# Optimization experiments

Measured on AMD Instinct MI355X. Metric: run time of the kernel, lower is better.

The kernel has to match this reference:

```python
import jax, jax.numpy as jnp
import numpy as np

EPS = 1e-5

def _ln(x, g, b):
    m = jnp.mean(x, axis=-1, keepdims=True)
    v = jnp.var(x, axis=-1, keepdims=True)
    return (x - m) / jnp.sqrt(v + EPS) * g + b

def setup_inputs() -> dict:
    key = jax.random.key(0)
    ks = jax.random.split(key, 16)
    B, T, N, K, d, E = 2, 12, 512, 8, 64, 64
    D = K * d
    s = 0.02
    inp = {
        "x": jax.random.normal(ks[0], (B, T, N, D), jnp.float32),
        "lapmatrix": jax.random.normal(ks[1], (N, N), jnp.float32),
        "node_embeddings": jax.random.normal(ks[2], (N, E), jnp.float32),
        "Wq": jax.random.normal(ks[3], (D, D), jnp.float32) * s,
        "bq": jnp.zeros((D,), jnp.float32),
        "Wk": jax.random.normal(ks[4], (D, D), jnp.float32) * s,
        "bk": jnp.zeros((D,), jnp.float32),
        "Wv": jax.random.normal(ks[5], (D, D), jnp.float32) * s,
        "bv": jnp.zeros((D,), jnp.float32),
        "Wo": jax.random.normal(ks[6], (D, D), jnp.float32) * s,
        "bo": jnp.zeros((D,), jnp.float32),
        "W1": jax.random.normal(ks[7], (4 * D, D), jnp.float32) * s,
        "b1": jnp.zeros((4 * D,), jnp.float32),
        "W2": jax.random.normal(ks[8], (D, 4 * D), jnp.float32) * s,
        "b2": jnp.zeros((D,), jnp.float32),
        "g1": jnp.ones((D,), jnp.float32),
        "be1": jnp.zeros((D,), jnp.float32),
        "g2": jnp.ones((D,), jnp.float32),
        "be2": jnp.zeros((D,), jnp.float32),
        "alpha": jnp.float32(1.0),
        "beta": jnp.float32(1.0),
        "k": 3,
    }
    return inp

def reference(x, lapmatrix, node_embeddings, Wq, bq, Wk, bk, Wv, bv, Wo, bo,
              W1, b1, W2, b2, g1, be1, g2, be2, alpha, beta, k):
    B, T, N, D = x.shape
    K, d = 8, D // 8
    x_raw = x
    xn = _ln(x, g1, be1)
    q = (xn @ Wq.T + bq).reshape(B, T, N, K, d)
    kk = (xn @ Wk.T + bk).reshape(B, T, N, K, d)
    v = (xn @ Wv.T + bv).reshape(B, T, N, K, d)
    # raw attention logits: [B,T,K,N,N]
    raw = jnp.einsum('btnkd,btmkd->btknm', q, kk) / jnp.sqrt(jnp.float32(d))
    # graph biases, all [N,N], broadcast over B,T,K
    supports = jax.nn.softmax(jax.nn.relu(node_embeddings @ node_embeddings.T), axis=1)
    adj = (lapmatrix != 0).astype(x.dtype)
    mask = jnp.where(adj == 0, jnp.float32(-1e9), jnp.float32(0.0))
    logits = raw + alpha * supports + beta * lapmatrix + mask
    attn = jax.nn.softmax(logits, axis=-1)  # dropout = identity in eval
    out = jnp.einsum('btknm,btmkd->btnkd', attn, v).reshape(B, T, N, D)
    x1 = x_raw + (out @ Wo.T + bo)
    h = _ln(x1, g2, be2)
    ffn = jax.nn.relu(h @ W1.T + b1) @ W2.T + b2
    return x1 + ffn
```

## Files before the change

kernel.cpp:

```cpp
#include <hip/hip_runtime.h>

typedef unsigned short u16;
typedef unsigned int   u32;
typedef __attribute__((ext_vector_type(8))) short bf16x8;
typedef __attribute__((ext_vector_type(4))) float f32x4;

#define DEV static __device__ __forceinline__

DEV float b2f(u16 u){ return __uint_as_float(((u32)u)<<16); }
DEV u16 f2b(float f){
  u32 u = __float_as_uint(f);
  u32 r = (u + 0x7FFFu + ((u>>16)&1u)) >> 16;
  return (u16)r;
}

union V8 { uint4 v; u16 s[8]; };

DEV u32 cvt_pk_bf16(float lo, float hi){
  u32 r;
  asm("v_cvt_pk_bf16_f32 %0, %1, %2" : "=v"(r) : "v"(lo), "v"(hi));
  return r;
}

DEV bool is_f32(const void* dt){ return *(const u32*)dt == 0x3F800000u; }

DEV uint4 ld8_ext_bf(const void* p, size_t i, bool f32){
  if(f32){
    const float* q = (const float*)p + i;
    float4 a = *(const float4*)q, b = *(const float4*)(q+4);
    V8 r;
    r.s[0]=f2b(a.x); r.s[1]=f2b(a.y); r.s[2]=f2b(a.z); r.s[3]=f2b(a.w);
    r.s[4]=f2b(b.x); r.s[5]=f2b(b.y); r.s[6]=f2b(b.z); r.s[7]=f2b(b.w);
    return r.v;
  }
  return *(const uint4*)((const u16*)p + i);
}
DEV void ld8_ext_f(const void* p, size_t i, bool f32, float* o){
  if(f32){
    const float* q = (const float*)p + i;
    float4 a = *(const float4*)q, b = *(const float4*)(q+4);
    o[0]=a.x;o[1]=a.y;o[2]=a.z;o[3]=a.w;o[4]=b.x;o[5]=b.y;o[6]=b.z;o[7]=b.w;
  }else{
    V8 u; u.v = *(const uint4*)((const u16*)p + i);
    #pragma unroll
    for(int k=0;k<8;k++) o[k]=b2f(u.s[k]);
  }
}
DEV float ld1_ext(const void* p, size_t i, bool f32){
  return f32 ? ((const float*)p)[i] : b2f(((const u16*)p)[i]);
}
DEV float load_scalar(const void* p, bool f32){
  return f32 ? *(const float*)p : b2f(*(const u16*)p);
}

DEV void gl_lds16(const u16* g, u16* l){
  __builtin_amdgcn_global_load_lds((const __attribute__((address_space(1))) void*)g,
                                   (__attribute__((address_space(3))) void*)l, 16, 0, 0);
}

__global__ __launch_bounds__(256) void sentinel_kernel(u16* out, long n, const void* dt){
  long ne = is_f32(dt) ? 2*n : n;
  long i = (long)blockIdx.x*256 + threadIdx.x;
  if(i < ne) out[i] = 0x4442;
}

__global__ __launch_bounds__(256) void prep_kernel(
    const void* __restrict__ x, const void* __restrict__ g1,
    const void* __restrict__ be1, u16* __restrict__ xn,
    const void* Wq, const void* Wk, const void* Wv, const void* Wo,
    const void* W1, const void* W2, u16* __restrict__ wbf,
    const void* bq, const void* bk, const void* bv, const void* bo,
    const void* b1, const void* b2, float* __restrict__ bfp,
    const void* __restrict__ E, const void* __restrict__ lap,
    const void* __restrict__ alpha_p, const void* __restrict__ beta_p,
    float* __restrict__ bm, const void* dt)
{
  __shared__ float En[64];
  __shared__ float red[8];
  const bool f32 = is_f32(dt);
  const int bid = blockIdx.x, t = threadIdx.x;

  if(bid < 3072){
    const int row = bid*4 + (t>>6), lane = t&63;
    float v[8];
    ld8_ext_f(x, (size_t)row*512 + lane*8, f32, v);
    float s=0.f, ss=0.f;
    #pragma unroll
    for(int i=0;i<8;i++){ s+=v[i]; ss+=v[i]*v[i]; }
    #pragma unroll
    for(int o=1;o<64;o<<=1){ s+=__shfl_xor(s,o,64); ss+=__shfl_xor(ss,o,64); }
    const float mean = s*(1.0f/512.0f);
    const float var  = ss*(1.0f/512.0f) - mean*mean;
    const float rstd = rsqrtf(var + 1e-5f);
    float gv[8], bv[8];
    ld8_ext_f(g1, (size_t)lane*8, f32, gv);
    ld8_ext_f(be1, (size_t)lane*8, f32, bv);
    V8 o8;
    #pragma unroll
    for(int i=0;i<8;i++) o8.s[i]=f2b((v[i]-mean)*rstd*gv[i]+bv[i]);
    *(uint4*)(xn+(size_t)row*512+lane*8)=o8.v;
  } else if(bid < 4608){
    size_t i = ((size_t)(bid-3072)*256 + t)*8;
    const void* src; size_t base;
    if(i < 262144){ src=Wq; base=0; }
    else if(i < 524288){ src=Wk; base=262144; }
    else if(i < 786432){ src=Wv; base=524288; }
    else if(i < 1048576){ src=Wo; base=786432; }
    else if(i < 2097152){ src=W1; base=1048576; }
    else { src=W2; base=2097152; }
    *(uint4*)(wbf + i) = ld8_ext_bf(src, i-base, f32);
  } else if(bid < 5120){
    const int n = bid - 4608;
    if(t < 64) En[t] = ld1_ext(E, (size_t)n*64 + t, f32);
    __syncthreads();
    const float alpha = load_scalar(alpha_p, f32);
    const float beta  = load_scalar(beta_p, f32);
    const int m0 = t, m1 = t+256;
    float sc0=0.f, sc1=0.f;
    #pragma unroll
    for(int c=0;c<8;c++){
      float a0[8], a1[8];
      ld8_ext_f(E, (size_t)m0*64 + c*8, f32, a0);
      ld8_ext_f(E, (size_t)m1*64 + c*8, f32, a1);
      #pragma unroll
      for(int j=0;j<8;j++){ const float en = En[c*8+j]; sc0 += en*a0[j]; sc1 += en*a1[j]; }
    }
    sc0 = fmaxf(sc0, 0.f); sc1 = fmaxf(sc1, 0.f);
    float mx = fmaxf(sc0, sc1);
    for(int o=1;o<64;o<<=1) mx = fmaxf(mx, __shfl_xor(mx,o,64));
    const int wave = t>>6;
    if((t&63)==0) red[wave]=mx;
    __syncthreads();
    mx = fmaxf(fmaxf(red[0],red[1]), fmaxf(red[2],red[3]));
    float e0 = __expf(sc0-mx), e1 = __expf(sc1-mx);
    float sm = e0+e1;
    for(int o=1;o<64;o<<=1) sm += __shfl_xor(sm,o,64);
    if((t&63)==0) red[4+wave]=sm;
    __syncthreads();
    sm = red[4]+red[5]+red[6]+red[7];
    const float inv = 1.f/sm;
    const int q0b = n>>5, iq = (n>>4)&1, l16 = n&15;
    const size_t qpart = (size_t)q0b*256 + (size_t)l16*4 + iq;
    float lv0 = ld1_ext(lap, (size_t)n*512+m0, f32);
    {
      float val = alpha*e0*inv + beta*lv0 + (lv0==0.f ? -1e9f : 0.f);
      int kb = m0>>3, e = m0&7;
      bm[(size_t)kb*4096 + qpart + (e>>1)*64 + (e&1)*2] = val;
    }
    float lv1 = ld1_ext(lap, (size_t)n*512+m1, f32);
    {
      float val = alpha*e1*inv + beta*lv1 + (lv1==0.f ? -1e9f : 0.f);
      int kb = m1>>3, e = m1&7;
      bm[(size_t)kb*4096 + qpart + (e>>1)*64 + (e&1)*2] = val;
    }
  } else {
    int j = (bid-5120)*256 + t;
    const void* src; int off;
    if(j < 512){ src=bq; off=0; }
    else if(j < 1024){ src=bk; off=512; }
    else if(j < 1536){ src=bv; off=1024; }
    else if(j < 2048){ src=bo; off=1536; }
    else if(j < 4096){ src=b1; off=2048; }
    else { src=b2; off=4096; }
    bfp[j] = ld1_ext(src, j-off, f32);
  }
}

template<int EXTIN>
__global__ __launch_bounds__(64) void ln_kernel(const void* __restrict__ xin,
    const void* __restrict__ g, const void* __restrict__ b, u16* __restrict__ out,
    const void* dt)
{
  const bool f32 = is_f32(dt);
  const int row = blockIdx.x, lane = threadIdx.x;
  float v[8];
  if(EXTIN){
    ld8_ext_f(xin, (size_t)row*512 + lane*8, f32, v);
  }else{
    V8 u; u.v = *(const uint4*)((const u16*)xin + (size_t)row*512 + lane*8);
    #pragma unroll
    for(int i=0;i<8;i++) v[i]=b2f(u.s[i]);
  }
  float s=0.f, ss=0.f;
  #pragma unroll
  for(int i=0;i<8;i++){ s+=v[i]; ss+=v[i]*v[i]; }
  #pragma unroll
  for(int o=1;o<64;o<<=1){ s+=__shfl_xor(s,o,64); ss+=__shfl_xor(ss,o,64); }
  const float mean = s*(1.0f/512.0f);
  const float var  = ss*(1.0f/512.0f) - mean*mean;
  const float rstd = rsqrtf(var + 1e-5f);
  float gv[8], bv[8];
  ld8_ext_f(g, (size_t)lane*8, f32, gv);
  ld8_ext_f(b, (size_t)lane*8, f32, bv);
  V8 o8;
  #pragma unroll
  for(int i=0;i<8;i++) o8.s[i]=f2b((v[i]-mean)*rstd*gv[i]+bv[i]);
  *(uint4*)(out+(size_t)row*512+lane*8)=o8.v;
}

template<int RELU, int RES, int RESEXT, int OUTEXT>
__global__ __launch_bounds__(256) void gemm_nt(
    const u16* __restrict__ A, const u16* __restrict__ B,
    const float* __restrict__ bias, const void* __restrict__ resid,
    void* __restrict__ Cout, int N, int K, const void* dt)
{
  __shared__ u16 As[128*64];
  __shared__ u16 Bs[128*64];
  const bool f32 = is_f32(dt);
  const int t = threadIdx.x;
  const int wave = t>>6, lane = t&63;
  const int n0 = blockIdx.y*128, m0 = blockIdx.x*128;
  const int wr = wave>>1, wc = wave&1;

  f32x4 acc[4][4];
  #pragma unroll
  for(int i=0;i<4;i++)
    #pragma unroll
    for(int j=0;j<4;j++){ acc[i][j][0]=0.f; acc[i][j][1]=0.f; acc[i][j][2]=0.f; acc[i][j][3]=0.f; }

  const int lrow8 = lane>>3, lg = lane&7;
  const int gsw = (lg ^ lrow8)*8;
  const u16* Ag = A + (size_t)(m0+lrow8)*K + gsw;
  const u16* Bg = B + (size_t)(n0+lrow8)*K + gsw;
  const int fr = lane&15, qd = lane>>4, frk = (fr&7);

  for(int k0=0; k0<K; k0+=64){
    __syncthreads();
    #pragma unroll
    for(int i=0;i<4;i++){
      int c = wave*4+i;
      gl_lds16(Ag + (size_t)(c*8)*K + k0, &As[c*512]);
      gl_lds16(Bg + (size_t)(c*8)*K + k0, &Bs[c*512]);
    }
    __syncthreads();
    #pragma unroll
    for(int s=0;s<2;s++){
      const int slot = ((s*4+qd) ^ frk)*8;
      bf16x8 af[4], bfr[4];
      #pragma unroll
      for(int i=0;i<4;i++) af[i] = *(const bf16x8*)&As[(wr*64+i*16+fr)*64 + slot];
      #pragma unroll
      for(int j=0;j<4;j++) bfr[j] = *(const bf16x8*)&Bs[(wc*64+j*16+fr)*64 + slot];
      #pragma unroll
      for(int i=0;i<4;i++)
        #pragma unroll
        for(int j=0;j<4;j++)
          acc[i][j] = __builtin_amdgcn_mfma_f32_16x16x32_bf16(af[i], bfr[j], acc[i][j], 0,0,0);
    }
  }

  const int col16 = lane&15, rbase = (lane>>4)*4;
  #pragma unroll
  for(int i=0;i<4;i++){
    #pragma unroll
    for(int j=0;j<4;j++){
      const int gc = n0 + wc*64 + j*16 + col16;
      const float bv = bias[gc];
      #pragma unroll
      for(int r=0;r<4;r++){
        const int gr = m0 + wr*64 + i*16 + rbase + r;
        float val = acc[i][j][r] + bv;
        if(RELU) val = fmaxf(val, 0.f);
        if(RES){
          if(RESEXT) val += ld1_ext(resid, (size_t)gr*N+gc, f32);
          else       val += b2f(((const u16*)resid)[(size_t)gr*N+gc]);
        }
        if(OUTEXT && f32) ((float*)Cout)[(size_t)gr*N+gc] = val;
        else              ((u16*)Cout)[(size_t)gr*N+gc] = f2b(val);
      }
    }
  }
}

template<int RELU, int RES, int RESEXT, int OUTEXT>
__global__ __launch_bounds__(256) void gemm_nt64(
    const u16* __restrict__ A, const u16* __restrict__ B,
    const float* __restrict__ bias, const void* __restrict__ resid,
    void* __restrict__ Cout, int N, int K, const void* dt)
{
  __shared__ u16 As[128*64];
  __shared__ u16 Bs[64*64];
  const bool f32 = is_f32(dt);
  const int t = threadIdx.x;
  const int wave = t>>6, lane = t&63;
  const int n0 = blockIdx.y*64, m0 = blockIdx.x*128;
  const int wr = wave>>1, wc = wave&1;

  f32x4 acc[4][2];
  #pragma unroll
  for(int i=0;i<4;i++)
    #pragma unroll
    for(int j=0;j<2;j++){ acc[i][j][0]=0.f; acc[i][j][1]=0.f; acc[i][j][2]=0.f; acc[i][j][3]=0.f; }

  const int lrow8 = lane>>3, lg = lane&7;
  const int gsw = (lg ^ lrow8)*8;
  const u16* Ag = A + (size_t)(m0+lrow8)*K + gsw;
  const u16* Bg = B + (size_t)(n0+lrow8)*K + gsw;
  const int fr = lane&15, qd = lane>>4, frk = (fr&7);

  for(int k0=0; k0<K; k0+=64){
    __syncthreads();
    #pragma unroll
    for(int i=0;i<4;i++){
      int c = wave*4+i;
      gl_lds16(Ag + (size_t)(c*8)*K + k0, &As[c*512]);
    }
    #pragma unroll
    for(int i=0;i<2;i++){
      int c = wave*2+i;
      gl_lds16(Bg + (size_t)(c*8)*K + k0, &Bs[c*512]);
    }
    __syncthreads();
    #pragma unroll
    for(int s=0;s<2;s++){
      const int slot = ((s*4+qd) ^ frk)*8;
      bf16x8 af[4], bfr[2];
      #pragma unroll
      for(int i=0;i<4;i++) af[i] = *(const bf16x8*)&As[(wr*64+i*16+fr)*64 + slot];
      #pragma unroll
      for(int j=0;j<2;j++) bfr[j] = *(const bf16x8*)&Bs[(wc*32+j*16+fr)*64 + slot];
      #pragma unroll
      for(int i=0;i<4;i++)
        #pragma unroll
        for(int j=0;j<2;j++)
          acc[i][j] = __builtin_amdgcn_mfma_f32_16x16x32_bf16(af[i], bfr[j], acc[i][j], 0,0,0);
    }
  }

  const int col16 = lane&15, rbase = (lane>>4)*4;
  #pragma unroll
  for(int i=0;i<4;i++){
    #pragma unroll
    for(int j=0;j<2;j++){
      const int gc = n0 + wc*32 + j*16 + col16;
      const float bv = bias[gc];
      #pragma unroll
      for(int r=0;r<4;r++){
        const int gr = m0 + wr*64 + i*16 + rbase + r;
        float val = acc[i][j][r] + bv;
        if(RELU) val = fmaxf(val, 0.f);
        if(RES){
          if(RESEXT) val += ld1_ext(resid, (size_t)gr*N+gc, f32);
          else       val += b2f(((const u16*)resid)[(size_t)gr*N+gc]);
        }
        if(OUTEXT && f32) ((float*)Cout)[(size_t)gr*N+gc] = val;
        else              ((u16*)Cout)[(size_t)gr*N+gc] = f2b(val);
      }
    }
  }
}

__global__ __launch_bounds__(256,3) void attn_kernel(
    const u16* __restrict__ qkv, const float* __restrict__ bm,
    u16* __restrict__ out)
{
  __shared__ u16 Kb[128*64];
  __shared__ u16 Vt[2][64*136];

  const int QS = 1536;
  const int t = threadIdx.x, wave = t>>6, lane = t&63;
  const int head = blockIdx.x, bt = blockIdx.z;
  const int q0 = blockIdx.y*128 + wave*32;
  const u16* qp = qkv + (size_t)bt*512*QS + head*64;
  const u16* kp = qp + 512;
  const u16* vp = qp + 1024;

  const int l16 = lane&15, qd = lane>>4;

  const int lrow8 = lane>>3, lg = lane&7;
  const int srow = t & 127;
  const int shalf = (t >> 7) * 32;
  const u16* vcp = vp + (size_t)srow*QS + shalf;

  #pragma unroll
  for(int ii=0;ii<4;ii++){
    const int c8 = wave*4 + ii;
    const int pg = lg ^ ((2*(lrow8&3) + (c8&3)) & 7);
    gl_lds16(kp + (size_t)(c8*8 + lrow8)*QS + pg*8, &Kb[c8*512]);
  }
  uint4 vv[4];
  #pragma unroll
  for(int qi=0;qi<4;qi++) vv[qi] = *(const uint4*)(vcp + qi*8);

  bf16x8 qf[2][2];
  #pragma unroll
  for(int i=0;i<2;i++)
    #pragma unroll
    for(int kc=0;kc<2;kc++)
      qf[i][kc] = *(const bf16x8*)(qp + (size_t)(q0 + i*16 + l16)*QS + kc*32 + qd*8);

  const float* bml = bm + (size_t)(blockIdx.y*4 + wave)*256 + (size_t)qd*4096 + (size_t)l16*4;

  const int arow = ((l16>>2)<<3) + (l16&3);
  const int rperm = (2*(l16&3) + (l16>>2)) & 7;
  const int g0 = (qd ^ rperm)*8;
  const u16* KA0 = &Kb[arow*64 + g0];
  const u16* KA1 = &Kb[arow*64 + (g0 ^ 32)];

  float mrun[2], lrun[2];
  mrun[0] = -3e38f; mrun[1] = -3e38f;
  lrun[0] = 0.f;    lrun[1] = 0.f;
  f32x4 oacc[2][4];
  #pragma unroll
  for(int i=0;i<2;i++)
    #pragma unroll
    for(int j=0;j<4;j++){ oacc[i][j][0]=0.f; oacc[i][j][1]=0.f; oacc[i][j][2]=0.f; oacc[i][j][3]=0.f; }

  #pragma unroll
  for(int qi=0;qi<4;qi++){
    V8 u; u.v = vv[qi];
    #pragma unroll
    for(int jj=0;jj<8;jj++) Vt[0][(shalf + qi*8 + jj)*136 + srow] = u.s[jj];
  }
  __syncthreads();

  #pragma unroll
  for(int c=0;c<4;c++){
    f32x4 p[2][8];
    __builtin_amdgcn_s_setprio(1);
    #pragma unroll
    for(int tt=0;tt<8;tt++){
      const int ro = (tt&3)*2048 + (tt>>2)*256;
      bf16x8 a0 = *(const bf16x8*)(KA0 + ro);
      bf16x8 a1 = *(const bf16x8*)(KA1 + ro);
      #pragma unroll
      for(int i=0;i<2;i++){
        f32x4 s; s[0]=0.f; s[1]=0.f; s[2]=0.f; s[3]=0.f;
        s = __builtin_amdgcn_mfma_f32_16x16x32_bf16(a0, qf[i][0], s, 0,0,0);
        s = __builtin_amdgcn_mfma_f32_16x16x32_bf16(a1, qf[i][1], s, 0,0,0);
        p[i][tt] = s;
      }
    }
    __builtin_amdgcn_s_setprio(0);
    if(c<3){
      __syncthreads();
      #pragma unroll
      for(int ii=0;ii<4;ii++){
        const int c8 = wave*4 + ii;
        const int pg = lg ^ ((2*(lrow8&3) + (c8&3)) & 7);
        gl_lds16(kp + (size_t)((c+1)*128 + c8*8 + lrow8)*QS + pg*8, &Kb[c8*512]);
      }
      #pragma unroll
      for(int qi=0;qi<4;qi++) vv[qi] = *(const uint4*)(vcp + (size_t)((c+1)*128)*QS + qi*8);
    }

    float mx0 = -3e38f, mx1 = -3e38f;
    #pragma unroll
    for(int s4=0;s4<4;s4++){
      const float* bp = bml + c*65536 + s4*16384;
      const float4 bg0 = *(const float4*)(bp);
      const float4 bg1 = *(const float4*)(bp + 64);
      const float4 bg2 = *(const float4*)(bp + 128);
      const float4 bg3 = *(const float4*)(bp + 192);
      #pragma unroll
      for(int i=0;i<2;i++){
        f32x4& pl = p[i][s4];
        pl[0] = pl[0]*0.125f + (i ? bg0.y : bg0.x);
        pl[1] = pl[1]*0.125f + (i ? bg0.w : bg0.z);
        pl[2] = pl[2]*0.125f + (i ? bg1.y : bg1.x);
        pl[3] = pl[3]*0.125f + (i ? bg1.w : bg1.z);
        f32x4& ph = p[i][s4+4];
        ph[0] = ph[0]*0.125f + (i ? bg2.y : bg2.x);
        ph[1] = ph[1]*0.125f + (i ? bg2.w : bg2.z);
        ph[2] = ph[2]*0.125f + (i ? bg3.y : bg3.x);
        ph[3] = ph[3]*0.125f + (i ? bg3.w : bg3.z);
        const float m8 = fmaxf(fmaxf(fmaxf(pl[0],pl[1]),fmaxf(pl[2],pl[3])),
                               fmaxf(fmaxf(ph[0],ph[1]),fmaxf(ph[2],ph[3])));
        if(i==0) mx0 = fmaxf(mx0, m8); else mx1 = fmaxf(mx1, m8);
      }
    }

    #pragma unroll
    for(int i=0;i<2;i++){
      float mx = i ? mx1 : mx0;
      mx = fmaxf(mx, __shfl_xor(mx, 16, 64));
      mx = fmaxf(mx, __shfl_xor(mx, 32, 64));
      const float mnew = fmaxf(mrun[i], mx);
      if(__any(mx > mrun[i])){
        const float al = __expf(mrun[i] - mnew);
        lrun[i] *= al;
        #pragma unroll
        for(int r=0;r<4;r++){
          const float alr = __shfl(al, (qd<<2)+r, 64);
          #pragma unroll
          for(int j=0;j<4;j++) oacc[i][j][r] *= alr;
        }
      }
      mrun[i] = mnew;
      float rs = 0.f;
      #pragma unroll
      for(int tt=0;tt<8;tt++){
        p[i][tt][0] = __expf(p[i][tt][0]-mnew);
        p[i][tt][1] = __expf(p[i][tt][1]-mnew);
        p[i][tt][2] = __expf(p[i][tt][2]-mnew);
        p[i][tt][3] = __expf(p[i][tt][3]-mnew);
        rs += (p[i][tt][0]+p[i][tt][1]) + (p[i][tt][2]+p[i][tt][3]);
      }
      rs += __shfl_xor(rs, 16, 64);
      rs += __shfl_xor(rs, 32, 64);
      lrun[i] += rs;
    }

    __builtin_amdgcn_s_setprio(1);
    #pragma unroll
    for(int ks=0;ks<4;ks++){
      union { bf16x8 v; u32 w[4]; } pa[2];
      #pragma unroll
      for(int i=0;i<2;i++){
        pa[i].w[0] = cvt_pk_bf16(p[i][ks][0],   p[i][ks][1]);
        pa[i].w[1] = cvt_pk_bf16(p[i][ks][2],   p[i][ks][3]);
        pa[i].w[2] = cvt_pk_bf16(p[i][ks+4][0], p[i][ks+4][1]);
        pa[i].w[3] = cvt_pk_bf16(p[i][ks+4][2], p[i][ks+4][3]);
      }
      #pragma unroll
      for(int j=0;j<4;j++){
        bf16x8 bvf = *(const bf16x8*)&Vt[c&1][(j*16 + l16)*136 + ks*32 + qd*8];
        oacc[0][j] = __builtin_amdgcn_mfma_f32_16x16x32_bf16(pa[0].v, bvf, oacc[0][j], 0,0,0);
        oacc[1][j] = __builtin_amdgcn_mfma_f32_16x16x32_bf16(pa[1].v, bvf, oacc[1][j], 0,0,0);
      }
    }
    __builtin_amdgcn_s_setprio(0);

    if(c<3){
      #pragma unroll
      for(int qi=0;qi<4;qi++){
        V8 u; u.v = vv[qi];
        #pragma unroll
        for(int jj=0;jj<8;jj++) Vt[(c+1)&1][(shalf + qi*8 + jj)*136 + srow] = u.s[jj];
      }
      __syncthreads();
    }
  }

  u16* op = out + (size_t)bt*512*512 + head*64;
  #pragma unroll
  for(int i=0;i<2;i++){
    const float inv = 1.f / lrun[i];
    #pragma unroll
    for(int r=0;r<4;r++){
      const float invr = __shfl(inv, (qd<<2)+r, 64);
      const size_t rowb = (size_t)(q0 + i*16 + qd*4 + r)*512;
      #pragma unroll
      for(int j=0;j<4;j++)
        op[rowb + j*16 + l16] = f2b(oacc[i][j][r] * invr);
    }
  }
}

extern "C" void kernel_launch(void* const* d_in, const int* in_sizes, int n_in,
                              void* d_out, int out_size, void* d_ws, size_t ws_size,
                              hipStream_t stream) {
  const void* x   = d_in[0];
  const void* lap = d_in[1];
  const void* ne  = d_in[2];
  const void* Wq  = d_in[3];
  const void* bq  = d_in[4];
  const void* Wk  = d_in[5];
  const void* bk  = d_in[6];
  const void* Wv  = d_in[7];
  const void* bv  = d_in[8];
  const void* Wo  = d_in[9];
  const void* bo  = d_in[10];
  const void* W1  = d_in[11];
  const void* b1  = d_in[12];
  const void* W2  = d_in[13];
  const void* b2  = d_in[14];
  const void* g1  = d_in[15];
  const void* be1 = d_in[16];
  const void* g2  = d_in[17];
  const void* be2 = d_in[18];
  const void* alpha = d_in[19];
  const void* beta  = d_in[20];
  const void* dt = g1;

  const int M = 12288;
  const size_t NEED = (size_t)512*512*4 + (size_t)M*512*2*2 + (size_t)M*2048*2
                    + (size_t)3145728*2 + (size_t)4608*4;
  if(ws_size < NEED){
    long n = out_size;
    sentinel_kernel<<<(2*n+255)/256, 256, 0, stream>>>((u16*)d_out, n, dt);
    return;
  }
  char* w = (char*)d_ws;
  float* bias_m = (float*)w;              w += (size_t)512*512*4;
  u16*   slotB  = (u16*)w;                w += (size_t)M*512*2;
  char*  slotC  = w;                      w += (size_t)M*2048*2;
  u16*   x1     = (u16*)w;                w += (size_t)M*512*2;
  u16*   wbf    = (u16*)w;                w += (size_t)3145728*2;
  float* bfp    = (float*)w;
  u16* qkv = (u16*)slotC;
  u16* h1  = (u16*)slotC;
  u16* xn = slotB;
  u16* ao = slotB;
  u16* h  = slotB;

  prep_kernel<<<5138, 256, 0, stream>>>(
      x, g1, be1, xn,
      Wq, Wk, Wv, Wo, W1, W2, wbf,
      bq, bk, bv, bo, b1, b2, bfp,
      ne, lap, alpha, beta, bias_m, dt);
  gemm_nt<0,0,0,0><<<dim3(96,12), 256, 0, stream>>>(xn, wbf, bfp, nullptr, qkv, 1536, 512, dt);
  attn_kernel<<<dim3(8,4,24), 256, 0, stream>>>(qkv, bias_m, ao);
  gemm_nt64<0,1,1,0><<<dim3(96,8), 256, 0, stream>>>(ao, wbf+786432, bfp+1536, x, x1, 512, 512, dt);
  ln_kernel<0><<<M, 64, 0, stream>>>(x1, g2, be2, h, dt);
  gemm_nt<1,0,0,0><<<dim3(96,16), 256, 0, stream>>>(h, wbf+1048576, bfp+2048, nullptr, h1, 2048, 512, dt);
  gemm_nt64<0,1,0,1><<<dim3(96,8), 256, 0, stream>>>(h1, wbf+2097152, bfp+4096, x1, d_out, 512, 2048, dt);
}
```

Before: 328.3 us.

## Double-buffer GEMM LDS tiles with K=32 steps and MFMA priority boost

```diff
diff --git a/kernel.cpp b/kernel.cpp
--- a/kernel.cpp
+++ b/kernel.cpp
@@ -204,8 +204,8 @@
     const float* __restrict__ bias, const void* __restrict__ resid,
     void* __restrict__ Cout, int N, int K, const void* dt)
 {
-  __shared__ u16 As[128*64];
-  __shared__ u16 Bs[128*64];
+  __shared__ u16 As[2][128*32];
+  __shared__ u16 Bs[2][128*32];
   const bool f32 = is_f32(dt);
   const int t = threadIdx.x;
   const int wave = t>>6, lane = t&63;
@@ -218,35 +218,51 @@
     #pragma unroll
     for(int j=0;j<4;j++){ acc[i][j][0]=0.f; acc[i][j][1]=0.f; acc[i][j][2]=0.f; acc[i][j][3]=0.f; }
 
-  const int lrow8 = lane>>3, lg = lane&7;
-  const int gsw = (lg ^ lrow8)*8;
-  const u16* Ag = A + (size_t)(m0+lrow8)*K + gsw;
-  const u16* Bg = B + (size_t)(n0+lrow8)*K + gsw;
-  const int fr = lane&15, qd = lane>>4, frk = (fr&7);
-
-  for(int k0=0; k0<K; k0+=64){
+  const int lrow16 = lane>>2, lg = lane&3;
+  const int pgsw = (lg ^ ((lrow16>>1)&3))*8;
+  const u16* Ag = A + (size_t)(m0+lrow16)*K + pgsw;
+  const u16* Bg = B + (size_t)(n0+lrow16)*K + pgsw;
+
+  const int fr = lane&15, qd = lane>>4;
+  const int slot = (qd ^ ((fr>>1)&3))*8;
+  const int aoff = (wr*64+fr)*32 + slot;
+  const int boff = (wc*64+fr)*32 + slot;
+
+  const int nt = K>>5;
+  #pragma unroll
+  for(int ii=0;ii<2;ii++){
+    const int c = wave*2+ii;
+    gl_lds16(Ag + (size_t)(c*16)*K, &As[0][c*512]);
+    gl_lds16(Bg + (size_t)(c*16)*K, &Bs[0][c*512]);
+  }
+  __syncthreads();
+
+  for(int tk=0; tk<nt; ++tk){
+    const int cur = tk&1;
+    if(tk+1 < nt){
+      const int k0 = (tk+1)*32;
+      #pragma unroll
+      for(int ii=0;ii<2;ii++){
+        const int c = wave*2+ii;
+        gl_lds16(Ag + (size_t)(c*16)*K + k0, &As[cur^1][c*512]);
+        gl_lds16(Bg + (size_t)(c*16)*K + k0, &Bs[cur^1][c*512]);
+      }
+    }
+    const u16* Ab = As[cur];
+    const u16* Bb = Bs[cur];
+    bf16x8 af[4], bfr[4];
+    #pragma unroll
+    for(int i=0;i<4;i++) af[i] = *(const bf16x8*)&Ab[aoff + i*512];
+    #pragma unroll
+    for(int j=0;j<4;j++) bfr[j] = *(const bf16x8*)&Bb[boff + j*512];
+    __builtin_amdgcn_s_setprio(1);
+    #pragma unroll
+    for(int i=0;i<4;i++)
+      #pragma unroll
+      for(int j=0;j<4;j++)
+        acc[i][j] = __builtin_amdgcn_mfma_f32_16x16x32_bf16(af[i], bfr[j], acc[i][j], 0,0,0);
+    __builtin_amdgcn_s_setprio(0);
     __syncthreads();
-    #pragma unroll
-    for(int i=0;i<4;i++){
-      int c = wave*4+i;
-      gl_lds16(Ag + (size_t)(c*8)*K + k0, &As[c*512]);
-      gl_lds16(Bg + (size_t)(c*8)*K + k0, &Bs[c*512]);
-    }
-    __syncthreads();
-    #pragma unroll
-    for(int s=0;s<2;s++){
-      const int slot = ((s*4+qd) ^ frk)*8;
-      bf16x8 af[4], bfr[4];
-      #pragma unroll
-      for(int i=0;i<4;i++) af[i] = *(const bf16x8*)&As[(wr*64+i*16+fr)*64 + slot];
-      #pragma unroll
-      for(int j=0;j<4;j++) bfr[j] = *(const bf16x8*)&Bs[(wc*64+j*16+fr)*64 + slot];
-      #pragma unroll
-      for(int i=0;i<4;i++)
-        #pragma unroll
-        for(int j=0;j<4;j++)
-          acc[i][j] = __builtin_amdgcn_mfma_f32_16x16x32_bf16(af[i], bfr[j], acc[i][j], 0,0,0);
-    }
   }
 
   const int col16 = lane&15, rbase = (lane>>4)*4;
@@ -278,8 +294,8 @@
     const float* __restrict__ bias, const void* __restrict__ resid,
     void* __restrict__ Cout, int N, int K, const void* dt)
 {
-  __shared__ u16 As[128*64];
-  __shared__ u16 Bs[64*64];
+  __shared__ u16 As[2][128*32];
+  __shared__ u16 Bs[2][64*32];
   const bool f32 = is_f32(dt);
   const int t = threadIdx.x;
   const int wave = t>>6, lane = t&63;
@@ -292,39 +308,51 @@
     #pragma unroll
     for(int j=0;j<2;j++){ acc[i][j][0]=0.f; acc[i][j][1]=0.f; acc[i][j][2]=0.f; acc[i][j][3]=0.f; }
 
-  const int lrow8 = lane>>3, lg = lane&7;
-  const int gsw = (lg ^ lrow8)*8;
-  const u16* Ag = A + (size_t)(m0+lrow8)*K + gsw;
-  const u16* Bg = B + (size_t)(n0+lrow8)*K + gsw;
-  const int fr = lane&15, qd = lane>>4, frk = (fr&7);
-
-  for(int k0=0; k0<K; k0+=64){
+  const int lrow16 = lane>>2, lg = lane&3;
+  const int pgsw = (lg ^ ((lrow16>>1)&3))*8;
+  const u16* Ag = A + (size_t)(m0+lrow16)*K + pgsw;
+  const u16* Bg = B + (size_t)(n0+lrow16)*K + pgsw;
+
+  const int fr = lane&15, qd = lane>>4;
+  const int slot = (qd ^ ((fr>>1)&3))*8;
+  const int aoff = (wr*64+fr)*32 + slot;
+  const int boff = (wc*32+fr)*32 + slot;
+
+  const int nt = K>>5;
+  #pragma unroll
+  for(int ii=0;ii<2;ii++){
+    const int c = wave*2+ii;
+    gl_lds16(Ag + (size_t)(c*16)*K, &As[0][c*512]);
+  }
+  gl_lds16(Bg + (size_t)(wave*16)*K, &Bs[0][wave*512]);
+  __syncthreads();
+
+  for(int tk=0; tk<nt; ++tk){
+    const int cur = tk&1;
+    if(tk+1 < nt){
+      const int k0 = (tk+1)*32;
+      #pragma unroll
+      for(int ii=0;ii<2;ii++){
+        const int c = wave*2+ii;
+        gl_lds16(Ag + (size_t)(c*16)*K + k0, &As[cur^1][c*512]);
+      }
+      gl_lds16(Bg + (size_t)(wave*16)*K + k0, &Bs[cur^1][wave*512]);
+    }
+    const u16* Ab = As[cur];
+    const u16* Bb = Bs[cur];
+    bf16x8 af[4], bfr[2];
+    #pragma unroll
+    for(int i=0;i<4;i++) af[i] = *(const bf16x8*)&Ab[aoff + i*512];
+    #pragma unroll
+    for(int j=0;j<2;j++) bfr[j] = *(const bf16x8*)&Bb[boff + j*512];
+    __builtin_amdgcn_s_setprio(1);
+    #pragma unroll
+    for(int i=0;i<4;i++)
+      #pragma unroll
+      for(int j=0;j<2;j++)
+        acc[i][j] = __builtin_amdgcn_mfma_f32_16x16x32_bf16(af[i], bfr[j], acc[i][j], 0,0,0);
+    __builtin_amdgcn_s_setprio(0);
     __syncthreads();
-    #pragma unroll
-    for(int i=0;i<4;i++){
-      int c = wave*4+i;
-      gl_lds16(Ag + (size_t)(c*8)*K + k0, &As[c*512]);
-    }
-    #pragma unroll
-    for(int i=0;i<2;i++){
-      int c = wave*2+i;
-      gl_lds16(Bg + (size_t)(c*8)*K + k0, &Bs[c*512]);
-    }
-    __syncthreads();
-    #pragma unroll
-    for(int s=0;s<2;s++){
-      const int slot = ((s*4+qd) ^ frk)*8;
-      bf16x8 af[4], bfr[2];
-      #pragma unroll
-      for(int i=0;i<4;i++) af[i] = *(const bf16x8*)&As[(wr*64+i*16+fr)*64 + slot];
-      #pragma unroll
-      for(int j=0;j<2;j++) bfr[j] = *(const bf16x8*)&Bs[(wc*32+j*16+fr)*64 + slot];
-      #pragma unroll
-      for(int i=0;i<4;i++)
-        #pragma unroll
-        for(int j=0;j<2;j++)
-          acc[i][j] = __builtin_amdgcn_mfma_f32_16x16x32_bf16(af[i], bfr[j], acc[i][j], 0,0,0);
-    }
   }
 
   const int col16 = lane&15, rbase = (lane>>4)*4;
```

After: 336.0 us. 2.3% more time.
